# Optimization experiments

Hardware: AMD Instinct MI355X
Metric: run time of the kernel (lower is better)

## Reference

```python
import jax, jax.numpy as jnp
import numpy as np

B, C, H_RES, W_RES = 8, 192, 64, 64


def dwconv(x, kern, pad):
    # depthwise conv, x: (B,C,H,W), kern: (C,1,k,k)
    return jax.lax.conv_general_dilated(
        x, kern, window_strides=(1, 1), padding=[(pad, pad), (pad, pad)],
        dimension_numbers=('NCHW', 'OIHW', 'NCHW'),
        feature_group_count=x.shape[1])


def omni_shift(x, alpha, dw1, dw3, dw5):
    # OmniShift (training branch): learnable mix of identity + depthwise 1x1/3x3/5x5
    return (alpha[0] * x + alpha[1] * dwconv(x, dw1, 0)
            + alpha[2] * dwconv(x, dw3, 1) + alpha[3] * dwconv(x, dw5, 2))


def biwkv(w, u, k, v):
    # Bidirectional WKV (Vision-RWKV style):
    # out_t = (sum_{i!=t} e^{-(|t-i|-1)w + k_i} v_i + e^{u+k_t} v_t)
    #       / (sum_{i!=t} e^{-(|t-i|-1)w + k_i}       + e^{u+k_t})
    # w,u: (C,); k,v: (B,T,C). Implemented as two stable log-scaled scans.
    kT = jnp.moveaxis(k, 1, 0)  # (T,B,C)
    vT = jnp.moveaxis(v, 1, 0)
    bc = (k.shape[0], k.shape[2])
    init = (jnp.full(bc, -jnp.inf, k.dtype), jnp.zeros(bc, k.dtype), jnp.zeros(bc, k.dtype))

    def step(carry, inp):
        p, num, den = carry          # state = e^p * (num, den) over strictly-previous tokens
        kt, vt = inp
        out = (p, num, den)          # emit BEFORE absorbing token t (i != t term)
        q = jnp.maximum(p - w, kt)
        e1 = jnp.exp(p - w - q)
        e2 = jnp.exp(kt - q)
        return (q, e1 * num + e2 * vt, e1 * den + e2), out

    _, (pf, nf, df) = jax.lax.scan(step, init, (kT, vT))
    _, (pb, nb, db) = jax.lax.scan(step, init, (kT[::-1], vT[::-1]))
    pb, nb, db = pb[::-1], nb[::-1], db[::-1]

    ps = u + kT                      # self term exponent
    r = jnp.maximum(jnp.maximum(pf, pb), ps)
    ef, eb, es = jnp.exp(pf - r), jnp.exp(pb - r), jnp.exp(ps - r)
    out = (ef * nf + eb * nb + es * vT) / (ef * df + eb * db + es)
    return jnp.moveaxis(out, 0, 1)   # (B,T,C)


def setup_inputs() -> dict:
    key = jax.random.key(0)
    ks = jax.random.split(key, 12)
    s = 1.0 / np.sqrt(C)
    inp = {
        'x': jax.random.normal(ks[0], (B, C, H_RES, W_RES), jnp.float32),
        'w_key': jax.random.normal(ks[1], (C, C), jnp.float32) * s,
        'w_value': jax.random.normal(ks[2], (C, C), jnp.float32) * s,
        'w_recept': jax.random.normal(ks[3], (C, C), jnp.float32) * s,
        'w_out': jax.random.normal(ks[4], (C, C), jnp.float32) * s,
        'decay': jax.random.normal(ks[5], (C,), jnp.float32),
        'boost': jax.random.normal(ks[6], (C,), jnp.float32),
        'alpha': jax.random.normal(ks[7], (4,), jnp.float32),
        'dw1': jax.random.normal(ks[8], (C, 1, 1, 1), jnp.float32) * s,
        'dw3': jax.random.normal(ks[9], (C, 1, 3, 3), jnp.float32) * (s / 3.0),
        'dw5': jax.random.normal(ks[10], (C, 1, 5, 5), jnp.float32) * (s / 5.0),
        'H': H_RES,
        'W': W_RES,
    }
    return inp


def reference(x, w_key, w_value, w_recept, w_out, decay, boost, alpha, dw1, dw3, dw5, H, W):
    Bn, Cn = x.shape[0], x.shape[1]
    T = H * W
    xs = omni_shift(x, alpha, dw1, dw3, dw5)                 # (B,C,H,W)
    xt = jnp.transpose(xs.reshape(Bn, Cn, T), (0, 2, 1))     # (B,T,C)
    k = jnp.einsum('btc,dc->btd', xt, w_key)
    v = jnp.einsum('btc,dc->btd', xt, w_value)
    sr = jax.nn.sigmoid(jnp.einsum('btc,dc->btd', xt, w_recept))
    y = biwkv(decay / T, boost / T, k, v)                    # (B,T,C)
    y = sr * y
    y = jnp.einsum('btd,cd->btc', y, w_out)
    return jnp.transpose(y, (0, 2, 1)).reshape(Bn, Cn, H, W)
```

## Files before the change

kernel.cpp:

```cpp
#include <hip/hip_runtime.h>
#include <math.h>

#define Cn 192
#define Bn 8
#define Tn 4096
#define HW 64

typedef unsigned short u16;
typedef unsigned int u32;
typedef __attribute__((ext_vector_type(8))) __bf16 bf16x8;
typedef __attribute__((ext_vector_type(16))) float f32x16;

__device__ __forceinline__ void gload16(const void* g, void* l) {
    __builtin_amdgcn_global_load_lds(
        (const __attribute__((address_space(1))) void*)g,
        (__attribute__((address_space(3))) void*)l, 16, 0, 0);
}

__device__ __forceinline__ void split_bf16(float x, u16 &h, u16 &l) {
    u32 u = __float_as_uint(x);
    u32 uh = (u + 0x7FFFu + ((u >> 16) & 1u)) & 0xFFFF0000u;
    h = (u16)(uh >> 16);
    float r = x - __uint_as_float(uh);
    u32 ur = __float_as_uint(r);
    l = (u16)((ur + 0x7FFFu + ((ur >> 16) & 1u)) >> 16);
}

__global__ __launch_bounds__(256) void omni_kernel(const float* __restrict__ x,
                                                   const float* __restrict__ alpha,
                                                   const float* __restrict__ dw1,
                                                   const float* __restrict__ dw3,
                                                   const float* __restrict__ dw5,
                                                   const float* __restrict__ Wk,
                                                   const float* __restrict__ Wv,
                                                   const float* __restrict__ Wr,
                                                   const float* __restrict__ Wo,
                                                   u16* __restrict__ xhi,
                                                   u16* __restrict__ xlo,
                                                   u16* __restrict__ wh,
                                                   u16* __restrict__ wl) {
    const int tid = threadIdx.x;
    if (blockIdx.x >= 1536) {
        const int base = (blockIdx.x - 1536) * 768;
        #pragma unroll
        for (int jj = 0; jj < 3; ++jj) {
            int idx = base + jj * 256 + tid;
            int mat = idx / 36864;
            int off = idx - mat * 36864;
            const float* src = (mat == 0) ? Wk : (mat == 1) ? Wv : (mat == 2) ? Wr : Wo;
            u16 h, l;
            split_bf16(src[off], h, l);
            wh[idx] = h;
            wl[idx] = l;
        }
        return;
    }

    const int plane = blockIdx.x;
    const int c = plane % Cn;
    const float* xin = x + (size_t)plane * Tn;
    u16* oh = xhi + (size_t)plane * Tn;
    u16* ol = xlo + (size_t)plane * Tn;

    __shared__ float tile[68 * 68];
    __shared__ float wk[25];

    if (tid == 0) {
        const float a0 = alpha[0], a1 = alpha[1], a2 = alpha[2], a3 = alpha[3];
        #pragma unroll
        for (int j = 0; j < 25; ++j) wk[j] = a3 * dw5[c * 25 + j];
        #pragma unroll
        for (int dy = 0; dy < 3; ++dy)
            #pragma unroll
            for (int dx = 0; dx < 3; ++dx)
                wk[(dy + 1) * 5 + (dx + 1)] += a2 * dw3[c * 9 + dy * 3 + dx];
        wk[12] += a1 * dw1[c] + a0;
    }
    for (int i = tid; i < 68 * 68; i += 256) {
        int r = i / 68, cc = i - r * 68;
        int gy = r - 2, gx = cc - 2;
        float v = 0.f;
        if (gy >= 0 && gy < HW && gx >= 0 && gx < HW) v = xin[gy * HW + gx];
        tile[i] = v;
    }
    __syncthreads();

    const int py = tid >> 3;
    const int px0 = (tid & 7) << 3;

    #pragma unroll
    for (int half = 0; half < 2; ++half) {
        const int y = py + half * 32;
        float row[5][12];
        #pragma unroll
        for (int dy = 0; dy < 5; ++dy) {
            const float4* rp = (const float4*)&tile[(y + dy) * 68 + px0];
            float4 r0 = rp[0], r1 = rp[1], r2 = rp[2];
            row[dy][0] = r0.x; row[dy][1] = r0.y; row[dy][2]  = r0.z; row[dy][3]  = r0.w;
            row[dy][4] = r1.x; row[dy][5] = r1.y; row[dy][6]  = r1.z; row[dy][7]  = r1.w;
            row[dy][8] = r2.x; row[dy][9] = r2.y; row[dy][10] = r2.z; row[dy][11] = r2.w;
        }
        u32 ph[4], pl[4];
        #pragma unroll
        for (int jj = 0; jj < 8; ++jj) {
            float acc = 0.f;
            #pragma unroll
            for (int dy = 0; dy < 5; ++dy)
                #pragma unroll
                for (int dx = 0; dx < 5; ++dx)
                    acc = fmaf(row[dy][jj + dx], wk[dy * 5 + dx], acc);
            u16 h, l2;
            split_bf16(acc, h, l2);
            if (jj & 1) { ph[jj >> 1] |= ((u32)h) << 16; pl[jj >> 1] |= ((u32)l2) << 16; }
            else        { ph[jj >> 1] = h;               pl[jj >> 1] = l2; }
        }
        *(uint4*)&oh[y * 64 + px0] = make_uint4(ph[0], ph[1], ph[2], ph[3]);
        *(uint4*)&ol[y * 64 + px0] = make_uint4(pl[0], pl[1], pl[2], pl[3]);
    }
}

__global__ __launch_bounds__(256) void transpose_kernel(const u16* __restrict__ ih,
                                                        const u16* __restrict__ il,
                                                        u16* __restrict__ oh,
                                                        u16* __restrict__ ol) {
    __shared__ u32 T[2][128][21];
    const int tid = threadIdx.x;
    const size_t ib = (size_t)blockIdx.z * Cn * Tn;
    const int c0 = blockIdx.y * 32, t0 = blockIdx.x * 128;

    {
        const int c2 = tid >> 4;
        const int tc = (tid & 15) * 8;
        const size_t ge = ib + (size_t)(c0 + 2 * c2) * Tn + t0 + tc;
        uint4 evh = *(const uint4*)&ih[ge];
        uint4 odh = *(const uint4*)&ih[ge + Tn];
        uint4 evl = *(const uint4*)&il[ge];
        uint4 odl = *(const uint4*)&il[ge + Tn];
        const u32 eh4[4] = {evh.x, evh.y, evh.z, evh.w};
        const u32 oh4[4] = {odh.x, odh.y, odh.z, odh.w};
        const u32 el4[4] = {evl.x, evl.y, evl.z, evl.w};
        const u32 ol4[4] = {odl.x, odl.y, odl.z, odl.w};
        #pragma unroll
        for (int q = 0; q < 4; ++q) {
            T[0][tc + 2 * q    ][c2] = (eh4[q] & 0xFFFFu) | (oh4[q] << 16);
            T[0][tc + 2 * q + 1][c2] = (eh4[q] >> 16) | (oh4[q] & 0xFFFF0000u);
            T[1][tc + 2 * q    ][c2] = (el4[q] & 0xFFFFu) | (ol4[q] << 16);
            T[1][tc + 2 * q + 1][c2] = (el4[q] >> 16) | (ol4[q] & 0xFFFF0000u);
        }
    }
    __syncthreads();
    {
        const int t = tid >> 1;
        const int hf = tid & 1;
        u32 wv[8][2];
        #pragma unroll
        for (int q = 0; q < 8; ++q) {
            wv[q][0] = T[0][t][hf * 8 + q];
            wv[q][1] = T[1][t][hf * 8 + q];
        }
        const size_t go = ib + (size_t)(t0 + t) * Cn + c0 + hf * 16;
        *(uint4*)&oh[go]     = make_uint4(wv[0][0], wv[1][0], wv[2][0], wv[3][0]);
        *(uint4*)&oh[go + 8] = make_uint4(wv[4][0], wv[5][0], wv[6][0], wv[7][0]);
        *(uint4*)&ol[go]     = make_uint4(wv[0][1], wv[1][1], wv[2][1], wv[3][1]);
        *(uint4*)&ol[go + 8] = make_uint4(wv[4][1], wv[5][1], wv[6][1], wv[7][1]);
    }
}

template<int NM>
__global__ __launch_bounds__(256) void gemm_mfma(const u16* __restrict__ wh,
                                                 const u16* __restrict__ wl,
                                                 const u16* __restrict__ Xh,
                                                 const u16* __restrict__ Xl,
                                                 float* __restrict__ O0,
                                                 float* __restrict__ O1,
                                                 float* __restrict__ O2,
                                                 int wrow0) {
    constexpr int ASZ = NM * 64 * 32;
    constexpr int BSZ = 128 * 32;
    __shared__ u16 Ah_[ASZ], Al_[ASZ];
    __shared__ u16 Bh_[BSZ], Bl_[BSZ];

    const int tid  = threadIdx.x;
    const int l    = tid & 63;
    const int wave = tid >> 6;
    const int wm   = wave >> 1, wn = wave & 1;
    const int m0   = blockIdx.y * 64;
    const int t0   = blockIdx.x * 128;
    const size_t xb = (size_t)blockIdx.z * Cn * Tn;

    f32x16 acc[NM][2];
    #pragma unroll
    for (int m = 0; m < NM; ++m)
        #pragma unroll
        for (int nf = 0; nf < 2; ++nf)
            #pragma unroll
            for (int r = 0; r < 16; ++r) acc[m][nf][r] = 0.f;

    auto stage = [&](int k0) {
        #pragma unroll
        for (int i = 0; i < NM; ++i) {
            int idx = i * 256 + tid;
            int row = idx >> 2;
            int cb  = (idx & 3) ^ ((row >> 1) & 3);
            int grow = wrow0 + (row >> 6) * 192 + m0 + (row & 63);
            int dst = (i * 256 + wave * 64) * 8;
            gload16(wh + (size_t)grow * Cn + k0 + cb * 8, Ah_ + dst);
            gload16(wl + (size_t)grow * Cn + k0 + cb * 8, Al_ + dst);
        }
        #pragma unroll
        for (int i = 0; i < 2; ++i) {
            int idx = i * 256 + tid;
            int tr  = idx >> 2;
            int cb  = (idx & 3) ^ ((tr >> 1) & 3);
            int dst = (i * 256 + wave * 64) * 8;
            gload16(Xh + xb + (size_t)(t0 + tr) * Cn + k0 + cb * 8, Bh_ + dst);
            gload16(Xl + xb + (size_t)(t0 + tr) * Cn + k0 + cb * 8, Bl_ + dst);
        }
    };

    auto compute = [&]() {
        #pragma unroll
        for (int kh = 0; kh < 2; ++kh) {
            const int cbb = kh * 2 + (l >> 5);
            bf16x8 ah[NM], al[NM];
            #pragma unroll
            for (int m = 0; m < NM; ++m) {
                int r = m * 64 + wm * 32 + (l & 31);
                int off = r * 32 + ((cbb ^ ((r >> 1) & 3)) << 3);
                ah[m] = *(const bf16x8*)&Ah_[off];
                al[m] = *(const bf16x8*)&Al_[off];
            }
            #pragma unroll
            for (int nf = 0; nf < 2; ++nf) {
                int tr = wn * 64 + nf * 32 + (l & 31);
                int off = tr * 32 + ((cbb ^ ((tr >> 1) & 3)) << 3);
                bf16x8 bh = *(const bf16x8*)&Bh_[off];
                bf16x8 bl = *(const bf16x8*)&Bl_[off];
                #pragma unroll
                for (int m = 0; m < NM; ++m) {
                    acc[m][nf] = __builtin_amdgcn_mfma_f32_32x32x16_bf16(ah[m], bh, acc[m][nf], 0, 0, 0);
                    acc[m][nf] = __builtin_amdgcn_mfma_f32_32x32x16_bf16(ah[m], bl, acc[m][nf], 0, 0, 0);
                    acc[m][nf] = __builtin_amdgcn_mfma_f32_32x32x16_bf16(al[m], bh, acc[m][nf], 0, 0, 0);
                }
            }
        }
    };

    stage(0);
    __syncthreads();
    for (int ks = 0; ks < 6; ++ks) {
        compute();
        if (ks < 5) {
            __syncthreads();
            stage((ks + 1) * 32);
            __syncthreads();
        }
    }

    float* Os[3] = {O0, O1, O2};
    #pragma unroll
    for (int m = 0; m < NM; ++m) {
        float* O = Os[m] + (size_t)blockIdx.z * Cn * Tn;
        #pragma unroll
        for (int nf = 0; nf < 2; ++nf) {
            int col = t0 + wn * 64 + nf * 32 + (l & 31);
            #pragma unroll
            for (int r = 0; r < 16; ++r) {
                int row = m0 + wm * 32 + (r & 3) + 8 * (r >> 2) + 4 * (l >> 5);
                O[(size_t)row * Tn + col] = acc[m][nf][r];
            }
        }
    }
}

__global__ __launch_bounds__(256) void wkv_kernel(const float* __restrict__ kg,
                                                  const float* __restrict__ vg,
                                                  const float* __restrict__ srlg,
                                                  const float* __restrict__ decay,
                                                  const float* __restrict__ boost,
                                                  u16* __restrict__ yhi,
                                                  u16* __restrict__ ylo) {
    const int row = blockIdx.x;
    const int d = row % Cn;
    const float* kr = kg + (size_t)row * Tn;
    const float* vr = vg + (size_t)row * Tn;
    const float* sr = srlg + (size_t)row * Tn;
    u16* yh = yhi + (size_t)row * Tn;
    u16* yl = ylo + (size_t)row * Tn;

    const int tid = threadIdx.x;
    const int t0 = tid * 16;

    float kk[16], vv[16];
    #pragma unroll
    for (int j = 0; j < 16; j += 4) {
        *(float4*)&kk[j] = *(const float4*)&kr[t0 + j];
        *(float4*)&vv[j] = *(const float4*)&vr[t0 + j];
    }

    __shared__ float red[256];
    float lm = kk[0];
    #pragma unroll
    for (int j = 1; j < 16; ++j) lm = fmaxf(lm, kk[j]);
    red[tid] = lm;
    __syncthreads();
    for (int s = 128; s > 0; s >>= 1) {
        if (tid < s) red[tid] = fmaxf(red[tid], red[tid + s]);
        __syncthreads();
    }
    const float m = red[0];
    __syncthreads();

    const float ww = decay[d] * (1.0f / (float)Tn);
    const float u = boost[d] * (1.0f / (float)Tn);
    const float lam = expf(-ww);
    const float lam16 = expf(-16.0f * ww);

    float a[16];
    #pragma unroll
    for (int j = 0; j < 16; ++j) a[j] = expf(kk[j] - m);

    float SN = 0.f, SD = 0.f;
    #pragma unroll
    for (int j = 0; j < 16; ++j) { SN = fmaf(lam, SN, a[j] * vv[j]); SD = fmaf(lam, SD, a[j]); }
    float BN = 0.f, BD = 0.f;
    #pragma unroll
    for (int j = 15; j >= 0; --j) { BN = fmaf(lam, BN, a[j] * vv[j]); BD = fmaf(lam, BD, a[j]); }

    __shared__ float sN[2][256], sD[2][256];

    sN[0][tid] = SN; sD[0][tid] = SD;
    __syncthreads();
    int src = 0;
    float f = lam16;
    for (int o = 1; o < 256; o <<= 1) {
        float nN = sN[src][tid], nD = sD[src][tid];
        if (tid >= o) { nN = fmaf(f, sN[src][tid - o], nN); nD = fmaf(f, sD[src][tid - o], nD); }
        sN[src ^ 1][tid] = nN; sD[src ^ 1][tid] = nD;
        __syncthreads();
        src ^= 1; f = f * f;
    }
    const float CfN = (tid > 0) ? sN[src][tid - 1] : 0.f;
    const float CfD = (tid > 0) ? sD[src][tid - 1] : 0.f;
    __syncthreads();

    sN[0][tid] = BN; sD[0][tid] = BD;
    __syncthreads();
    src = 0; f = lam16;
    for (int o = 1; o < 256; o <<= 1) {
        float nN = sN[src][tid], nD = sD[src][tid];
        if (tid + o < 256) { nN = fmaf(f, sN[src][tid + o], nN); nD = fmaf(f, sD[src][tid + o], nD); }
        sN[src ^ 1][tid] = nN; sD[src ^ 1][tid] = nD;
        __syncthreads();
        src ^= 1; f = f * f;
    }
    const float CbN = (tid < 255) ? sN[src][tid + 1] : 0.f;
    const float CbD = (tid < 255) ? sD[src][tid + 1] : 0.f;

    float fN[16], fD[16];
    float cN = CfN, cD = CfD;
    #pragma unroll
    for (int j = 0; j < 16; ++j) {
        fN[j] = cN; fD[j] = cD;
        cN = fmaf(lam, cN, a[j] * vv[j]);
        cD = fmaf(lam, cD, a[j]);
    }

    float sl[16];
    #pragma unroll
    for (int j = 0; j < 16; j += 4) *(float4*)&sl[j] = *(const float4*)&sr[t0 + j];

    u16 oh[16], ol[16];
    float bN = CbN, bD = CbD;
    #pragma unroll
    for (int j = 15; j >= 0; --j) {
        const float es = expf(u + kk[j] - m);
        const float num = fN[j] + bN + es * vv[j];
        const float den = fD[j] + bD + es;
        const float y = num / den;
        const float sig = 1.0f / (1.0f + expf(-sl[j]));
        split_bf16(sig * y, oh[j], ol[j]);
        bN = fmaf(lam, bN, a[j] * vv[j]);
        bD = fmaf(lam, bD, a[j]);
    }

    u32 ph[8], pl[8];
    #pragma unroll
    for (int j = 0; j < 8; ++j) {
        ph[j] = (u32)oh[2 * j] | ((u32)oh[2 * j + 1] << 16);
        pl[j] = (u32)ol[2 * j] | ((u32)ol[2 * j + 1] << 16);
    }
    *(uint4*)&yh[t0]     = make_uint4(ph[0], ph[1], ph[2], ph[3]);
    *(uint4*)&yh[t0 + 8] = make_uint4(ph[4], ph[5], ph[6], ph[7]);
    *(uint4*)&yl[t0]     = make_uint4(pl[0], pl[1], pl[2], pl[3]);
    *(uint4*)&yl[t0 + 8] = make_uint4(pl[4], pl[5], pl[6], pl[7]);
}

extern "C" void kernel_launch(void* const* d_in, const int* in_sizes, int n_in,
                              void* d_out, int out_size, void* d_ws, size_t ws_size,
                              hipStream_t stream) {
    const float* x        = (const float*)d_in[0];
    const float* w_key    = (const float*)d_in[1];
    const float* w_value  = (const float*)d_in[2];
    const float* w_recept = (const float*)d_in[3];
    const float* w_out    = (const float*)d_in[4];
    const float* decay    = (const float*)d_in[5];
    const float* boost    = (const float*)d_in[6];
    const float* alpha    = (const float*)d_in[7];
    const float* dw1      = (const float*)d_in[8];
    const float* dw3      = (const float*)d_in[9];
    const float* dw5      = (const float*)d_in[10];

    const size_t S = (size_t)Bn * Cn * Tn;
    u16* R0 = (u16*)d_ws;
    u16* R1 = R0 + 2 * S;
    u16* R2 = R1 + 2 * S;
    u16* whp = R2 + 2 * S;
    u16* wlp = whp + 4 * 36864;

    u16* xs_hi = R0;        u16* xs_lo = R0 + S;
    u16* Xt_hi = R1;        u16* Xt_lo = R1 + S;
    float* kb  = (float*)R0;
    float* vb  = (float*)R2;
    float* srl = (float*)d_out;
    u16* y_hi  = R1;        u16* y_lo  = R1 + S;
    u16* Yt_hi = R2;        u16* Yt_lo = R2 + S;
    float* out = (float*)d_out;

    omni_kernel<<<dim3(1536 + 192), 256, 0, stream>>>(x, alpha, dw1, dw3, dw5,
                                                      w_key, w_value, w_recept, w_out,
                                                      xs_hi, xs_lo, whp, wlp);

    transpose_kernel<<<dim3(32, 6, 8), 256, 0, stream>>>(xs_hi, xs_lo, Xt_hi, Xt_lo);

    gemm_mfma<3><<<dim3(32, 3, 8), 256, 0, stream>>>(whp, wlp, Xt_hi, Xt_lo, kb, vb, srl, 0);

    wkv_kernel<<<dim3(Bn * Cn), 256, 0, stream>>>(kb, vb, srl, decay, boost, y_hi, y_lo);

    transpose_kernel<<<dim3(32, 6, 8), 256, 0, stream>>>(y_hi, y_lo, Yt_hi, Yt_lo);

    gemm_mfma<1><<<dim3(32, 3, 8), 256, 0, stream>>>(whp, wlp, Yt_hi, Yt_lo, out, nullptr, nullptr, 576);
}
```

Before: 121.9 us.

## Fuse transposes into GEMM staging and WKV output into final projection

```diff
diff --git a/kernel.cpp b/kernel.cpp
--- a/kernel.cpp
+++ b/kernel.cpp
@@ -119,66 +119,15 @@
     }
 }
 
-__global__ __launch_bounds__(256) void transpose_kernel(const u16* __restrict__ ih,
-                                                        const u16* __restrict__ il,
-                                                        u16* __restrict__ oh,
-                                                        u16* __restrict__ ol) {
-    __shared__ u32 T[2][128][21];
-    const int tid = threadIdx.x;
-    const size_t ib = (size_t)blockIdx.z * Cn * Tn;
-    const int c0 = blockIdx.y * 32, t0 = blockIdx.x * 128;
-
-    {
-        const int c2 = tid >> 4;
-        const int tc = (tid & 15) * 8;
-        const size_t ge = ib + (size_t)(c0 + 2 * c2) * Tn + t0 + tc;
-        uint4 evh = *(const uint4*)&ih[ge];
-        uint4 odh = *(const uint4*)&ih[ge + Tn];
-        uint4 evl = *(const uint4*)&il[ge];
-        uint4 odl = *(const uint4*)&il[ge + Tn];
-        const u32 eh4[4] = {evh.x, evh.y, evh.z, evh.w};
-        const u32 oh4[4] = {odh.x, odh.y, odh.z, odh.w};
-        const u32 el4[4] = {evl.x, evl.y, evl.z, evl.w};
-        const u32 ol4[4] = {odl.x, odl.y, odl.z, odl.w};
-        #pragma unroll
-        for (int q = 0; q < 4; ++q) {
-            T[0][tc + 2 * q    ][c2] = (eh4[q] & 0xFFFFu) | (oh4[q] << 16);
-            T[0][tc + 2 * q + 1][c2] = (eh4[q] >> 16) | (oh4[q] & 0xFFFF0000u);
-            T[1][tc + 2 * q    ][c2] = (el4[q] & 0xFFFFu) | (ol4[q] << 16);
-            T[1][tc + 2 * q + 1][c2] = (el4[q] >> 16) | (ol4[q] & 0xFFFF0000u);
-        }
-    }
-    __syncthreads();
-    {
-        const int t = tid >> 1;
-        const int hf = tid & 1;
-        u32 wv[8][2];
-        #pragma unroll
-        for (int q = 0; q < 8; ++q) {
-            wv[q][0] = T[0][t][hf * 8 + q];
-            wv[q][1] = T[1][t][hf * 8 + q];
-        }
-        const size_t go = ib + (size_t)(t0 + t) * Cn + c0 + hf * 16;
-        *(uint4*)&oh[go]     = make_uint4(wv[0][0], wv[1][0], wv[2][0], wv[3][0]);
-        *(uint4*)&oh[go + 8] = make_uint4(wv[4][0], wv[5][0], wv[6][0], wv[7][0]);
-        *(uint4*)&ol[go]     = make_uint4(wv[0][1], wv[1][1], wv[2][1], wv[3][1]);
-        *(uint4*)&ol[go + 8] = make_uint4(wv[4][1], wv[5][1], wv[6][1], wv[7][1]);
-    }
-}
-
-template<int NM>
-__global__ __launch_bounds__(256) void gemm_mfma(const u16* __restrict__ wh,
+__global__ __launch_bounds__(256) void gemm_proj(const u16* __restrict__ wh,
                                                  const u16* __restrict__ wl,
                                                  const u16* __restrict__ Xh,
                                                  const u16* __restrict__ Xl,
                                                  float* __restrict__ O0,
                                                  float* __restrict__ O1,
-                                                 float* __restrict__ O2,
-                                                 int wrow0) {
-    constexpr int ASZ = NM * 64 * 32;
-    constexpr int BSZ = 128 * 32;
-    __shared__ u16 Ah_[ASZ], Al_[ASZ];
-    __shared__ u16 Bh_[BSZ], Bl_[BSZ];
+                                                 float* __restrict__ O2) {
+    __shared__ u16 Ah_[3 * 64 * 32], Al_[3 * 64 * 32];
+    __shared__ u16 Bh_[128 * 36], Bl_[128 * 36];
 
     const int tid  = threadIdx.x;
     const int l    = tid & 63;
@@ -187,44 +136,61 @@
     const int m0   = blockIdx.y * 64;
     const int t0   = blockIdx.x * 128;
     const size_t xb = (size_t)blockIdx.z * Cn * Tn;
-
-    f32x16 acc[NM][2];
-    #pragma unroll
-    for (int m = 0; m < NM; ++m)
+    const int cpair = tid & 15;
+    const int toct  = tid >> 4;
+
+    f32x16 acc[3][2];
+    #pragma unroll
+    for (int m = 0; m < 3; ++m)
         #pragma unroll
         for (int nf = 0; nf < 2; ++nf)
             #pragma unroll
             for (int r = 0; r < 16; ++r) acc[m][nf][r] = 0.f;
 
-    auto stage = [&](int k0) {
-        #pragma unroll
-        for (int i = 0; i < NM; ++i) {
+    uint4 rh0, rh1, rl0, rl1;
+
+    auto loadB = [&](int k0) {
+        size_t g = xb + (size_t)(k0 + 2 * cpair) * Tn + t0 + toct * 8;
+        rh0 = *(const uint4*)&Xh[g];
+        rh1 = *(const uint4*)&Xh[g + Tn];
+        rl0 = *(const uint4*)&Xl[g];
+        rl1 = *(const uint4*)&Xl[g + Tn];
+    };
+    auto writeB = [&]() {
+        const u32 h0[4] = {rh0.x, rh0.y, rh0.z, rh0.w};
+        const u32 h1[4] = {rh1.x, rh1.y, rh1.z, rh1.w};
+        const u32 l0[4] = {rl0.x, rl0.y, rl0.z, rl0.w};
+        const u32 l1[4] = {rl1.x, rl1.y, rl1.z, rl1.w};
+        #pragma unroll
+        for (int j = 0; j < 8; ++j) {
+            int t = toct * 8 + j;
+            int sh = 16 * (j & 1);
+            u32 a = (h0[j >> 1] >> sh) & 0xFFFFu;
+            u32 b = (h1[j >> 1] >> sh) & 0xFFFFu;
+            *(u32*)&Bh_[t * 36 + 2 * cpair] = a | (b << 16);
+            u32 c = (l0[j >> 1] >> sh) & 0xFFFFu;
+            u32 d = (l1[j >> 1] >> sh) & 0xFFFFu;
+            *(u32*)&Bl_[t * 36 + 2 * cpair] = c | (d << 16);
+        }
+    };
+    auto stageA = [&](int k0) {
+        #pragma unroll
+        for (int i = 0; i < 3; ++i) {
             int idx = i * 256 + tid;
             int row = idx >> 2;
             int cb  = (idx & 3) ^ ((row >> 1) & 3);
-            int grow = wrow0 + (row >> 6) * 192 + m0 + (row & 63);
-            int dst = (i * 256 + wave * 64) * 8;
-            gload16(wh + (size_t)grow * Cn + k0 + cb * 8, Ah_ + dst);
-            gload16(wl + (size_t)grow * Cn + k0 + cb * 8, Al_ + dst);
-        }
-        #pragma unroll
-        for (int i = 0; i < 2; ++i) {
-            int idx = i * 256 + tid;
-            int tr  = idx >> 2;
-            int cb  = (idx & 3) ^ ((tr >> 1) & 3);
-            int dst = (i * 256 + wave * 64) * 8;
-            gload16(Xh + xb + (size_t)(t0 + tr) * Cn + k0 + cb * 8, Bh_ + dst);
-            gload16(Xl + xb + (size_t)(t0 + tr) * Cn + k0 + cb * 8, Bl_ + dst);
+            int grow = (row >> 6) * 192 + m0 + (row & 63);
+            gload16(wh + (size_t)grow * Cn + k0 + cb * 8, Ah_ + idx * 8);
+            gload16(wl + (size_t)grow * Cn + k0 + cb * 8, Al_ + idx * 8);
         }
     };
-
     auto compute = [&]() {
         #pragma unroll
         for (int kh = 0; kh < 2; ++kh) {
             const int cbb = kh * 2 + (l >> 5);
-            bf16x8 ah[NM], al[NM];
-            #pragma unroll
-            for (int m = 0; m < NM; ++m) {
+            bf16x8 ah[3], al[3];
+            #pragma unroll
+            for (int m = 0; m < 3; ++m) {
                 int r = m * 64 + wm * 32 + (l & 31);
                 int off = r * 32 + ((cbb ^ ((r >> 1) & 3)) << 3);
                 ah[m] = *(const bf16x8*)&Ah_[off];
@@ -232,34 +198,42 @@
             }
             #pragma unroll
             for (int nf = 0; nf < 2; ++nf) {
-                int tr = wn * 64 + nf * 32 + (l & 31);
-                int off = tr * 32 + ((cbb ^ ((tr >> 1) & 3)) << 3);
-                bf16x8 bh = *(const bf16x8*)&Bh_[off];
-                bf16x8 bl = *(const bf16x8*)&Bl_[off];
+                int t = wn * 64 + nf * 32 + (l & 31);
+                int o = t * 36 + cbb * 8;
+                union { uint2 q[2]; bf16x8 v; } th, tl2;
+                th.q[0]  = *(const uint2*)&Bh_[o];
+                th.q[1]  = *(const uint2*)&Bh_[o + 4];
+                tl2.q[0] = *(const uint2*)&Bl_[o];
+                tl2.q[1] = *(const uint2*)&Bl_[o + 4];
                 #pragma unroll
-                for (int m = 0; m < NM; ++m) {
-                    acc[m][nf] = __builtin_amdgcn_mfma_f32_32x32x16_bf16(ah[m], bh, acc[m][nf], 0, 0, 0);
-                    acc[m][nf] = __builtin_amdgcn_mfma_f32_32x32x16_bf16(ah[m], bl, acc[m][nf], 0, 0, 0);
-                    acc[m][nf] = __builtin_amdgcn_mfma_f32_32x32x16_bf16(al[m], bh, acc[m][nf], 0, 0, 0);
+                for (int m = 0; m < 3; ++m) {
+                    acc[m][nf] = __builtin_amdgcn_mfma_f32_32x32x16_bf16(ah[m], th.v,  acc[m][nf], 0, 0, 0);
+                    acc[m][nf] = __builtin_amdgcn_mfma_f32_32x32x16_bf16(ah[m], tl2.v, acc[m][nf], 0, 0, 0);
+                    acc[m][nf] = __builtin_amdgcn_mfma_f32_32x32x16_bf16(al[m], th.v,  acc[m][nf], 0, 0, 0);
                 }
             }
         }
     };
 
-    stage(0);
-    __syncthreads();
+    loadB(0);
+    stageA(0);
+    writeB();
+    __syncthreads();
+    loadB(32);
     for (int ks = 0; ks < 6; ++ks) {
         compute();
         if (ks < 5) {
             __syncthreads();
-            stage((ks + 1) * 32);
+            writeB();
+            stageA((ks + 1) * 32);
             __syncthreads();
+            if (ks < 4) loadB((ks + 2) * 32);
         }
     }
 
     float* Os[3] = {O0, O1, O2};
     #pragma unroll
-    for (int m = 0; m < NM; ++m) {
+    for (int m = 0; m < 3; ++m) {
         float* O = Os[m] + (size_t)blockIdx.z * Cn * Tn;
         #pragma unroll
         for (int nf = 0; nf < 2; ++nf) {
@@ -273,20 +247,14 @@
     }
 }
 
-__global__ __launch_bounds__(256) void wkv_kernel(const float* __restrict__ kg,
-                                                  const float* __restrict__ vg,
-                                                  const float* __restrict__ srlg,
-                                                  const float* __restrict__ decay,
-                                                  const float* __restrict__ boost,
-                                                  u16* __restrict__ yhi,
-                                                  u16* __restrict__ ylo) {
+__global__ __launch_bounds__(256) void wkv_stats(const float* __restrict__ kg,
+                                                 const float* __restrict__ vg,
+                                                 const float* __restrict__ decay,
+                                                 float4* __restrict__ states) {
     const int row = blockIdx.x;
     const int d = row % Cn;
     const float* kr = kg + (size_t)row * Tn;
     const float* vr = vg + (size_t)row * Tn;
-    const float* sr = srlg + (size_t)row * Tn;
-    u16* yh = yhi + (size_t)row * Tn;
-    u16* yl = ylo + (size_t)row * Tn;
 
     const int tid = threadIdx.x;
     const int t0 = tid * 16;
@@ -298,27 +266,13 @@
         *(float4*)&vv[j] = *(const float4*)&vr[t0 + j];
     }
 
-    __shared__ float red[256];
-    float lm = kk[0];
-    #pragma unroll
-    for (int j = 1; j < 16; ++j) lm = fmaxf(lm, kk[j]);
-    red[tid] = lm;
-    __syncthreads();
-    for (int s = 128; s > 0; s >>= 1) {
-        if (tid < s) red[tid] = fmaxf(red[tid], red[tid + s]);
-        __syncthreads();
-    }
-    const float m = red[0];
-    __syncthreads();
-
     const float ww = decay[d] * (1.0f / (float)Tn);
-    const float u = boost[d] * (1.0f / (float)Tn);
     const float lam = expf(-ww);
     const float lam16 = expf(-16.0f * ww);
 
     float a[16];
     #pragma unroll
-    for (int j = 0; j < 16; ++j) a[j] = expf(kk[j] - m);
+    for (int j = 0; j < 16; ++j) a[j] = expf(kk[j]);
 
     float SN = 0.f, SD = 0.f;
     #pragma unroll
@@ -357,43 +311,136 @@
     const float CbN = (tid < 255) ? sN[src][tid + 1] : 0.f;
     const float CbD = (tid < 255) ? sD[src][tid + 1] : 0.f;
 
-    float fN[16], fD[16];
-    float cN = CfN, cD = CfD;
-    #pragma unroll
-    for (int j = 0; j < 16; ++j) {
-        fN[j] = cN; fD[j] = cD;
-        cN = fmaf(lam, cN, a[j] * vv[j]);
-        cD = fmaf(lam, cD, a[j]);
-    }
-
-    float sl[16];
-    #pragma unroll
-    for (int j = 0; j < 16; j += 4) *(float4*)&sl[j] = *(const float4*)&sr[t0 + j];
-
-    u16 oh[16], ol[16];
-    float bN = CbN, bD = CbD;
-    #pragma unroll
-    for (int j = 15; j >= 0; --j) {
-        const float es = expf(u + kk[j] - m);
-        const float num = fN[j] + bN + es * vv[j];
-        const float den = fD[j] + bD + es;
-        const float y = num / den;
-        const float sig = 1.0f / (1.0f + expf(-sl[j]));
-        split_bf16(sig * y, oh[j], ol[j]);
-        bN = fmaf(lam, bN, a[j] * vv[j]);
-        bD = fmaf(lam, bD, a[j]);
-    }
-
-    u32 ph[8], pl[8];
-    #pragma unroll
-    for (int j = 0; j < 8; ++j) {
-        ph[j] = (u32)oh[2 * j] | ((u32)oh[2 * j + 1] << 16);
-        pl[j] = (u32)ol[2 * j] | ((u32)ol[2 * j + 1] << 16);
-    }
-    *(uint4*)&yh[t0]     = make_uint4(ph[0], ph[1], ph[2], ph[3]);
-    *(uint4*)&yh[t0 + 8] = make_uint4(ph[4], ph[5], ph[6], ph[7]);
-    *(uint4*)&yl[t0]     = make_uint4(pl[0], pl[1], pl[2], pl[3]);
-    *(uint4*)&yl[t0 + 8] = make_uint4(pl[4], pl[5], pl[6], pl[7]);
+    const int b = row / Cn;
+    states[((size_t)(b * 256 + tid)) * Cn + d] = make_float4(CfN, CfD, CbN, CbD);
+}
+
+__global__ __launch_bounds__(512) void wkv_out(const float* __restrict__ kb,
+                                               const float* __restrict__ vb,
+                                               const float* __restrict__ srl,
+                                               const float4* __restrict__ states,
+                                               const float* __restrict__ decay,
+                                               const float* __restrict__ boost,
+                                               const u16* __restrict__ wh,
+                                               const u16* __restrict__ wl,
+                                               float* __restrict__ out) {
+    __shared__ u16 Yh_[128 * 196], Yl_[128 * 196];
+    __shared__ u16 Ah_[192 * 32], Al_[192 * 32];
+
+    const int tid = threadIdx.x;
+    const int b = blockIdx.y;
+    const int t0 = blockIdx.x * 128;
+
+    for (int pass = 0; pass < 3; ++pass) {
+        const int task = pass * 512 + tid;
+        const int d  = task % Cn;
+        const int ch = task / Cn;
+        const size_t rbase = ((size_t)b * Cn + d) * Tn + t0 + ch * 16;
+        const float4 st = states[((size_t)(b * 256 + (t0 >> 4) + ch)) * Cn + d];
+        const float ww = decay[d] * (1.0f / (float)Tn);
+        const float lam = expf(-ww);
+        const float u = boost[d] * (1.0f / (float)Tn);
+
+        float kk[16], vv[16], sl[16];
+        #pragma unroll
+        for (int j = 0; j < 16; j += 4) {
+            *(float4*)&kk[j] = *(const float4*)&kb[rbase + j];
+            *(float4*)&vv[j] = *(const float4*)&vb[rbase + j];
+            *(float4*)&sl[j] = *(const float4*)&srl[rbase + j];
+        }
+        float a[16];
+        #pragma unroll
+        for (int j = 0; j < 16; ++j) a[j] = expf(kk[j]);
+
+        float fN[16], fD[16];
+        float cN = st.x, cD = st.y;
+        #pragma unroll
+        for (int j = 0; j < 16; ++j) {
+            fN[j] = cN; fD[j] = cD;
+            cN = fmaf(lam, cN, a[j] * vv[j]);
+            cD = fmaf(lam, cD, a[j]);
+        }
+        float bN = st.z, bD = st.w;
+        #pragma unroll
+        for (int j = 15; j >= 0; --j) {
+            const float es = expf(u + kk[j]);
+            const float y = (fN[j] + bN + es * vv[j]) / (fD[j] + bD + es);
+            const float sig = 1.0f / (1.0f + expf(-sl[j]));
+            u16 h, l2;
+            split_bf16(sig * y, h, l2);
+            const int t = ch * 16 + j;
+            Yh_[t * 196 + d] = h;
+            Yl_[t * 196 + d] = l2;
+            bN = fmaf(lam, bN, a[j] * vv[j]);
+            bD = fmaf(lam, bD, a[j]);
+        }
+    }
+    __syncthreads();
+
+    const int l = tid & 63;
+    const int wave = tid >> 6;
+    const int wm = wave >> 2;
+    const int wn = wave & 3;
+
+    f32x16 acc[3];
+    #pragma unroll
+    for (int mf = 0; mf < 3; ++mf)
+        #pragma unroll
+        for (int r = 0; r < 16; ++r) acc[mf][r] = 0.f;
+
+    for (int ks = 0; ks < 6; ++ks) {
+        {
+            int idx = tid;
+            int row = idx >> 2;
+            int cb = (idx & 3) ^ ((row >> 1) & 3);
+            gload16(wh + (size_t)(576 + row) * Cn + ks * 32 + cb * 8, Ah_ + idx * 8);
+            gload16(wl + (size_t)(576 + row) * Cn + ks * 32 + cb * 8, Al_ + idx * 8);
+            if (tid < 256) {
+                idx = 512 + tid;
+                row = idx >> 2;
+                cb = (idx & 3) ^ ((row >> 1) & 3);
+                gload16(wh + (size_t)(576 + row) * Cn + ks * 32 + cb * 8, Ah_ + idx * 8);
+                gload16(wl + (size_t)(576 + row) * Cn + ks * 32 + cb * 8, Al_ + idx * 8);
+            }
+        }
+        __syncthreads();
+        #pragma unroll
+        for (int kh = 0; kh < 2; ++kh) {
+            const int cbb = kh * 2 + (l >> 5);
+            bf16x8 ah[3], al[3];
+            #pragma unroll
+            for (int mf = 0; mf < 3; ++mf) {
+                int r = wm * 96 + mf * 32 + (l & 31);
+                int off = r * 32 + ((cbb ^ ((r >> 1) & 3)) << 3);
+                ah[mf] = *(const bf16x8*)&Ah_[off];
+                al[mf] = *(const bf16x8*)&Al_[off];
+            }
+            const int t = wn * 32 + (l & 31);
+            const int o = t * 196 + ks * 32 + cbb * 8;
+            union { uint2 q[2]; bf16x8 v; } bh, bl;
+            bh.q[0] = *(const uint2*)&Yh_[o];
+            bh.q[1] = *(const uint2*)&Yh_[o + 4];
+            bl.q[0] = *(const uint2*)&Yl_[o];
+            bl.q[1] = *(const uint2*)&Yl_[o + 4];
+            #pragma unroll
+            for (int mf = 0; mf < 3; ++mf) {
+                acc[mf] = __builtin_amdgcn_mfma_f32_32x32x16_bf16(ah[mf], bh.v, acc[mf], 0, 0, 0);
+                acc[mf] = __builtin_amdgcn_mfma_f32_32x32x16_bf16(ah[mf], bl.v, acc[mf], 0, 0, 0);
+                acc[mf] = __builtin_amdgcn_mfma_f32_32x32x16_bf16(al[mf], bh.v, acc[mf], 0, 0, 0);
+            }
+        }
+        __syncthreads();
+    }
+
+    #pragma unroll
+    for (int mf = 0; mf < 3; ++mf) {
+        const int col = t0 + wn * 32 + (l & 31);
+        #pragma unroll
+        for (int r = 0; r < 16; ++r) {
+            int row = wm * 96 + mf * 32 + (r & 3) + 8 * (r >> 2) + 4 * (l >> 5);
+            out[((size_t)b * Cn + row) * Tn + col] = acc[mf][r];
+        }
+    }
 }
 
 extern "C" void kernel_launch(void* const* d_in, const int* in_sizes, int n_in,
@@ -419,25 +466,20 @@
     u16* wlp = whp + 4 * 36864;
 
     u16* xs_hi = R0;        u16* xs_lo = R0 + S;
-    u16* Xt_hi = R1;        u16* Xt_lo = R1 + S;
-    float* kb  = (float*)R0;
+    float* kb  = (float*)R1;
     float* vb  = (float*)R2;
     float* srl = (float*)d_out;
-    u16* y_hi  = R1;        u16* y_lo  = R1 + S;
-    u16* Yt_hi = R2;        u16* Yt_lo = R2 + S;
+    float4* states = (float4*)R0;
     float* out = (float*)d_out;
 
     omni_kernel<<<dim3(1536 + 192), 256, 0, stream>>>(x, alpha, dw1, dw3, dw5,
                                                       w_key, w_value, w_recept, w_out,
                                                       xs_hi, xs_lo, whp, wlp);
 
-    transpose_kernel<<<dim3(32, 6, 8), 256, 0, stream>>>(xs_hi, xs_lo, Xt_hi, Xt_lo);
-
-    gemm_mfma<3><<<dim3(32, 3, 8), 256, 0, stream>>>(whp, wlp, Xt_hi, Xt_lo, kb, vb, srl, 0);
-
-    wkv_kernel<<<dim3(Bn * Cn), 256, 0, stream>>>(kb, vb, srl, decay, boost, y_hi, y_lo);
-
-    transpose_kernel<<<dim3(32, 6, 8), 256, 0, stream>>>(y_hi, y_lo, Yt_hi, Yt_lo);
-
-    gemm_mfma<1><<<dim3(32, 3, 8), 256, 0, stream>>>(whp, wlp, Yt_hi, Yt_lo, out, nullptr, nullptr, 576);
-}
+    gemm_proj<<<dim3(32, 3, 8), 256, 0, stream>>>(whp, wlp, xs_hi, xs_lo, kb, vb, srl);
+
+    wkv_stats<<<dim3(Bn * Cn), 256, 0, stream>>>(kb, vb, decay, states);
+
+    wkv_out<<<dim3(32, 8), 512, 0, stream>>>(kb, vb, srl, states, decay, boost,
+                                             whp, wlp, out);
+}
```

After: 107.9 us. 11.5% less time.
